# Performance work log

Hardware: AMD Instinct MI355X
Metric: run time of the kernel (lower is better)

Reference implementation:

```python
import jax, jax.numpy as jnp
import numpy as np

N = 4096
NFEAT = 1024
NHID = 512
NCLS = 32
NLAYERS = 3
SPARSITY = 0.002


def _l2norm(x, eps=1e-12):
    n = jnp.sqrt(jnp.sum(x * x, axis=1, keepdims=True))
    return x / jnp.maximum(n, eps)


def setup_inputs() -> dict:
    key = jax.random.key(0)
    ks = jax.random.split(key, 12)
    # sparse-valued dense adjacency (original stores torch.sparse but densifies every hop)
    vals = jax.random.uniform(ks[0], (N, N), dtype=jnp.float32)
    mask = jax.random.uniform(ks[1], (N, N)) < SPARSITY
    adj = jnp.where(mask, vals, 0.0)
    features = jax.random.normal(ks[2], (N, NFEAT), dtype=jnp.float32)
    # y is a one-hot label matrix [N, nclass]
    labels = jax.random.randint(ks[3], (N,), 0, NCLS)
    y = jax.nn.one_hot(labels, NCLS, dtype=jnp.float32)
    s = 0.02
    W0 = jax.random.normal(ks[4], (NFEAT + 3 * NCLS, NHID), dtype=jnp.float32) * s
    b0 = jnp.zeros((NHID,), jnp.float32)
    W1_0 = jax.random.normal(ks[5], (NHID + 3 * NCLS, NHID), dtype=jnp.float32) * s
    b1_0 = jnp.zeros((NHID,), jnp.float32)
    W1_1 = jax.random.normal(ks[6], (NHID + 3 * NCLS, NHID), dtype=jnp.float32) * s
    b1_1 = jnp.zeros((NHID,), jnp.float32)
    W2 = jax.random.normal(ks[7], (NFEAT + NHID, NCLS), dtype=jnp.float32) * s
    b2 = jnp.zeros((NCLS,), jnp.float32)
    alphas = jnp.ones((NLAYERS, 5), jnp.float32)
    return {
        "adj": adj, "features": features, "y": y,
        "W0": W0, "b0": b0, "W1_0": W1_0, "b1_0": b1_0,
        "W1_1": W1_1, "b1_1": b1_1, "W2": W2, "b2": b2,
        "alphas": alphas, "layer_norm": 1,
    }


def reference(adj, features, y, W0, b0, W1_0, b1_0, W1_1, b1_1, W2, b2, alphas, layer_norm):
    Ws = [(W0, b0), (W1_0, b1_0), (W1_1, b1_1)]
    initial_features = jax.lax.stop_gradient(features)  # .clone().detach()
    feats = features
    max_features = None
    pow_adj = adj  # persists across layers (faithful to original): hops adj, adj^2, adj^4
    for i in range(NLAYERS):
        mask_alpha = jax.nn.softmax(alphas[i], axis=0)
        for _ in range(i):
            pow_adj = adj @ pow_adj
        hop = pow_adj @ feats                                   # [N, d]
        dist = (pow_adj > 0).astype(adj.dtype)                  # binarized reachability
        y_out = dist @ y                                        # [N, c]
        y_in = dist.T @ y                                       # [N, c]
        y_all = y_in + y_out
        hop = mask_alpha[0] * hop
        y_out = mask_alpha[1] * y_out
        y_in = mask_alpha[2] * y_in
        y_all = mask_alpha[3] * y_all
        mat = jnp.concatenate([hop, y_out, y_in, y_all], axis=1)
        W, b = Ws[i]
        tmp = mat @ W + b
        if layer_norm:
            tmp = _l2norm(tmp)
        feats = tmp
        max_features = tmp if max_features is None else jnp.maximum(max_features, tmp)
    final_mat = jnp.concatenate([initial_features, max_features], axis=1)
    out = jax.nn.relu(final_mat)
    # dropout: eval mode (identity)
    out = out @ W2 + b2
    return jax.nn.log_softmax(out, axis=1)
```

## Files before the change

kernel.cpp:

```cpp
#include <hip/hip_runtime.h>
#include <hip/hip_bf16.h>
#include <math.h>

typedef unsigned long long u64;
typedef unsigned short ushort_t;
typedef float f32x4 __attribute__((ext_vector_type(4)));
typedef short s16x8 __attribute__((ext_vector_type(8)));

#define NN 4096
#define NF 1024
#define NH 512
#define NC 32
#define LDP 40

__device__ inline float bf2f(ushort_t u) {
    unsigned int v = ((unsigned int)u) << 16;
    return __uint_as_float(v);
}
__device__ inline ushort_t f2bf(float f) {
    __hip_bfloat16 h = __float2bfloat16(f);
    return *(ushort_t*)&h;
}

__device__ void role_build(int i, int l, const float* __restrict__ adj,
                           u64* __restrict__ B1, int* __restrict__ rowcnt,
                           int* __restrict__ colidx, float* __restrict__ vals) {
    const float* row = adj + (size_t)i * NN + l * 64;
    const float4* row4 = (const float4*)row;
    u64 w = 0;
    #pragma unroll
    for (int k = 0; k < 16; ++k) {
        float4 v = row4[k];
        if (v.x > 0.f) w |= 1ULL << (4*k + 0);
        if (v.y > 0.f) w |= 1ULL << (4*k + 1);
        if (v.z > 0.f) w |= 1ULL << (4*k + 2);
        if (v.w > 0.f) w |= 1ULL << (4*k + 3);
    }
    B1[(size_t)i*64 + l] = w;
    int cnt = __popcll(w);
    int pre = cnt;
    #pragma unroll
    for (int o = 1; o < 64; o <<= 1) {
        int u = __shfl_up(pre, o, 64);
        if (l >= o) pre += u;
    }
    int excl = pre - cnt;
    int total = __shfl(pre, 63, 64);
    u64 ww = w;
    int idx = excl;
    while (ww) {
        int b = __ffsll((unsigned long long)ww) - 1;
        ww &= ww - 1;
        if (idx < 64) {
            colidx[i*64 + idx] = l*64 + b;
            vals[i*64 + idx] = row[b];
        }
        ++idx;
    }
    int tot = total < 64 ? total : 64;
    for (int s = tot + l; s < 64; s += 64) {
        colidx[i*64 + s] = 0;
        vals[i*64 + s] = 0.f;
    }
    if (l == 0) {
        int r8 = (tot + 7) & ~7;
        rowcnt[i] = r8 < 64 ? r8 : 64;
    }
}

__device__ void role_wt(const float* __restrict__ W, ushort_t* __restrict__ Wt,
                        int ksrc0, int Kd, int idx, char* smem, int t) {
    float (*tile)[33] = (float(*)[33])smem;
    int ktiles = Kd >> 5;
    int kb = (idx % ktiles) * 32, nb = (idx / ktiles) * 32;
    int tc = t & 31, tr8 = t >> 5;
    for (int r = tr8; r < 32; r += 8)
        tile[r][tc] = W[(size_t)(ksrc0 + kb + r) * NH + nb + tc];
    __syncthreads();
    for (int r = tr8; r < 32; r += 8)
        Wt[(size_t)(nb + r) * Kd + kb + tc] = f2bf(tile[tc][r]);
}

__device__ void role_bsq(int i, int t, char* smem, const u64* __restrict__ Bidx,
                         const u64* __restrict__ Bdat, u64* __restrict__ Bout) {
    u64* ridx = (u64*)smem;
    u64* part = ridx + 64;
    int wid = t >> 6, lane = t & 63;
    if (t < 64) ridx[t] = Bidx[(size_t)i*64 + t];
    __syncthreads();
    u64 acc = 0;
    for (int u = wid*16; u < wid*16 + 16; ++u) {
        u64 w = ridx[u];
        while (w) {
            int k = u*64 + (__ffsll((unsigned long long)w) - 1);
            w &= (w - 1);
            acc |= Bdat[(size_t)k*64 + lane];
        }
    }
    part[wid*64 + lane] = acc;
    __syncthreads();
    if (t < 64) Bout[(size_t)i*64 + t] = part[t] | part[64+t] | part[128+t] | part[192+t];
}

__device__ void role_btrans(int tb, int wid, int l, char* smem,
                            const u64* __restrict__ B, u64* __restrict__ BT) {
    u64* ld = ((u64*)smem) + wid*64;
    int I = tb >> 6, J = tb & 63;
    ld[l] = B[(size_t)(I*64 + l)*64 + J];
    __syncthreads();
    u64 out = 0;
    #pragma unroll
    for (int r = 0; r < 64; ++r) out |= ((ld[r] >> l) & 1ULL) << r;
    BT[(size_t)(J*64 + l)*64 + I] = out;
}

__device__ void role_ymat(int rb, int t, char* smem, const u64* __restrict__ B,
                          const u64* __restrict__ BT, const u64* __restrict__ LC,
                          const float* __restrict__ asp, ushort_t* __restrict__ yc) {
    u64* LCt   = (u64*)smem;
    u64* rows  = LCt + 64*32;
    u64* rowsT = rows + 8*64;
    for (int k = t; k < 2048; k += 256) {
        int c = k >> 6, w = k & 63;
        LCt[w*32 + c] = LC[k];
    }
    for (int k = t; k < 512; k += 256) {
        int r = k >> 6, w = k & 63;
        rows[r*64 + w]  = B[(size_t)(rb + r)*64 + w];
        rowsT[r*64 + w] = BT[(size_t)(rb + r)*64 + w];
    }
    __syncthreads();
    int wid = t >> 6, lane = t & 63;
    int h = lane >> 5, c = lane & 31;
    int r = wid * 2 + h;
    int co = 0, ci = 0;
    #pragma unroll
    for (int w = 0; w < 64; ++w) {
        u64 lc = LCt[w*32 + c];
        co += __popcll(rows[r*64 + w]  & lc);
        ci += __popcll(rowsT[r*64 + w] & lc);
    }
    float a1 = asp[1], a2 = asp[2], a3 = asp[3];
    size_t i = rb + r;
    yc[i*96 + c]      = f2bf(a1 * (float)co);
    yc[i*96 + 32 + c] = f2bf(a2 * (float)ci);
    yc[i*96 + 64 + c] = f2bf(a3 * (float)(co + ci));
}

__device__ void role_gemm(int bx, int tid, char* smem, const ushort_t* __restrict__ Abf,
                          const float* __restrict__ Af, int Ka,
                          const ushort_t* __restrict__ Bt, int K,
                          ushort_t* __restrict__ Cb, float* __restrict__ Cf) {
    ushort_t* As = (ushort_t*)smem;
    ushort_t* Bs = As + 64*LDP;
    int xcd = bx & 7, rest = bx >> 3;
    int nt = rest & 7, mt = (rest >> 3) * 8 + xcd;
    int bm = mt * 64, bn = nt * 64;
    int srow = tid >> 2, scol = (tid & 3) * 8;
    int wid = tid >> 6, lane = tid & 63;
    int fr = lane & 15, hi2 = lane >> 4, fk = hi2 * 8;
    f32x4 acc[4] = {{0,0,0,0},{0,0,0,0},{0,0,0,0},{0,0,0,0}};
    for (int k0 = 0; k0 < K; k0 += 32) {
        if (Abf) {
            *(s16x8*)&As[srow * LDP + scol] =
                *(const s16x8*)&Abf[(size_t)(bm + srow) * Ka + k0 + scol];
        } else {
            const float* ap = &Af[(size_t)(bm + srow) * Ka + k0 + scol];
            float4 a0 = *(const float4*)ap;
            float4 a1 = *(const float4*)(ap + 4);
            s16x8 o;
            o[0] = (short)f2bf(a0.x); o[1] = (short)f2bf(a0.y);
            o[2] = (short)f2bf(a0.z); o[3] = (short)f2bf(a0.w);
            o[4] = (short)f2bf(a1.x); o[5] = (short)f2bf(a1.y);
            o[6] = (short)f2bf(a1.z); o[7] = (short)f2bf(a1.w);
            *(s16x8*)&As[srow * LDP + scol] = o;
        }
        *(s16x8*)&Bs[srow * LDP + scol] =
            *(const s16x8*)&Bt[(size_t)(bn + srow) * K + k0 + scol];
        __syncthreads();
        s16x8 af = *(const s16x8*)&As[(wid * 16 + fr) * LDP + fk];
        #pragma unroll
        for (int j = 0; j < 4; ++j) {
            s16x8 bfv = *(const s16x8*)&Bs[(j * 16 + fr) * LDP + fk];
            acc[j] = __builtin_amdgcn_mfma_f32_16x16x32_bf16(af, bfv, acc[j], 0, 0, 0);
        }
        __syncthreads();
    }
    int drow = bm + wid * 16 + hi2 * 4;
    #pragma unroll
    for (int j = 0; j < 4; ++j) {
        int col = bn + j * 16 + fr;
        #pragma unroll
        for (int r = 0; r < 4; ++r) {
            if (Cb) Cb[(size_t)(drow + r) * NH + col] = f2bf(acc[j][r]);
            else    Cf[(size_t)(drow + r) * NH + col] = acc[j][r];
        }
    }
}

__device__ void role_spmm(int i, int lane, const int* __restrict__ rc,
                          const int* __restrict__ ci, const float* __restrict__ vl,
                          const ushort_t* __restrict__ X, ushort_t* __restrict__ Y) {
    int cnt = rc[i];
    float acc[8] = {0,0,0,0,0,0,0,0};
    for (int p = 0; p < cnt; p += 8) {
        int4   c0 = *(const int4*)&ci[i*64 + p];
        int4   c1 = *(const int4*)&ci[i*64 + p + 4];
        float4 v0 = *(const float4*)&vl[i*64 + p];
        float4 v1 = *(const float4*)&vl[i*64 + p + 4];
        s16x8 x0 = *(const s16x8*)&X[(size_t)c0.x * NH + 8*lane];
        s16x8 x1 = *(const s16x8*)&X[(size_t)c0.y * NH + 8*lane];
        s16x8 x2 = *(const s16x8*)&X[(size_t)c0.z * NH + 8*lane];
        s16x8 x3 = *(const s16x8*)&X[(size_t)c0.w * NH + 8*lane];
        s16x8 x4 = *(const s16x8*)&X[(size_t)c1.x * NH + 8*lane];
        s16x8 x5 = *(const s16x8*)&X[(size_t)c1.y * NH + 8*lane];
        s16x8 x6 = *(const s16x8*)&X[(size_t)c1.z * NH + 8*lane];
        s16x8 x7 = *(const s16x8*)&X[(size_t)c1.w * NH + 8*lane];
        #pragma unroll
        for (int j = 0; j < 8; ++j) {
            acc[j] += v0.x * bf2f((ushort_t)x0[j]);
            acc[j] += v0.y * bf2f((ushort_t)x1[j]);
            acc[j] += v0.z * bf2f((ushort_t)x2[j]);
            acc[j] += v0.w * bf2f((ushort_t)x3[j]);
            acc[j] += v1.x * bf2f((ushort_t)x4[j]);
            acc[j] += v1.y * bf2f((ushort_t)x5[j]);
            acc[j] += v1.z * bf2f((ushort_t)x6[j]);
            acc[j] += v1.w * bf2f((ushort_t)x7[j]);
        }
    }
    s16x8 o;
    #pragma unroll
    for (int j = 0; j < 8; ++j) o[j] = (short)f2bf(acc[j]);
    *(s16x8*)&Y[(size_t)i*NH + 8*lane] = o;
}

__device__ void role_spmmF(int i, int lane, const int* __restrict__ rc,
                           const int* __restrict__ ci, const float* __restrict__ vl,
                           const ushort_t* __restrict__ X, const float* __restrict__ yv,
                           const float* __restrict__ bias, int ln, float alpha,
                           ushort_t* __restrict__ F) {
    int cnt = rc[i];
    float acc[8] = {0,0,0,0,0,0,0,0};
    for (int p = 0; p < cnt; p += 8) {
        int4   c0 = *(const int4*)&ci[i*64 + p];
        int4   c1 = *(const int4*)&ci[i*64 + p + 4];
        float4 v0 = *(const float4*)&vl[i*64 + p];
        float4 v1 = *(const float4*)&vl[i*64 + p + 4];
        s16x8 x0 = *(const s16x8*)&X[(size_t)c0.x * NH + 8*lane];
        s16x8 x1 = *(const s16x8*)&X[(size_t)c0.y * NH + 8*lane];
        s16x8 x2 = *(const s16x8*)&X[(size_t)c0.z * NH + 8*lane];
        s16x8 x3 = *(const s16x8*)&X[(size_t)c0.w * NH + 8*lane];
        s16x8 x4 = *(const s16x8*)&X[(size_t)c1.x * NH + 8*lane];
        s16x8 x5 = *(const s16x8*)&X[(size_t)c1.y * NH + 8*lane];
        s16x8 x6 = *(const s16x8*)&X[(size_t)c1.z * NH + 8*lane];
        s16x8 x7 = *(const s16x8*)&X[(size_t)c1.w * NH + 8*lane];
        #pragma unroll
        for (int j = 0; j < 8; ++j) {
            acc[j] += v0.x * bf2f((ushort_t)x0[j]);
            acc[j] += v0.y * bf2f((ushort_t)x1[j]);
            acc[j] += v0.z * bf2f((ushort_t)x2[j]);
            acc[j] += v0.w * bf2f((ushort_t)x3[j]);
            acc[j] += v1.x * bf2f((ushort_t)x4[j]);
            acc[j] += v1.y * bf2f((ushort_t)x5[j]);
            acc[j] += v1.z * bf2f((ushort_t)x6[j]);
            acc[j] += v1.w * bf2f((ushort_t)x7[j]);
        }
    }
    const float* yr = yv + (size_t)i * NH + 8*lane;
    float4 ya = *(const float4*)yr;
    float4 yb = *(const float4*)(yr + 4);
    float4 ba = *(const float4*)&bias[8*lane];
    float4 bb = *(const float4*)&bias[8*lane + 4];
    float v[8];
    v[0] = alpha*acc[0] + ya.x + ba.x; v[1] = alpha*acc[1] + ya.y + ba.y;
    v[2] = alpha*acc[2] + ya.z + ba.z; v[3] = alpha*acc[3] + ya.w + ba.w;
    v[4] = alpha*acc[4] + yb.x + bb.x; v[5] = alpha*acc[5] + yb.y + bb.y;
    v[6] = alpha*acc[6] + yb.z + bb.z; v[7] = alpha*acc[7] + yb.w + bb.w;
    float ss = 0.f;
    #pragma unroll
    for (int j = 0; j < 8; ++j) ss += v[j]*v[j];
    #pragma unroll
    for (int o = 1; o < 64; o <<= 1) ss += __shfl_xor(ss, o, 64);
    float sc = ln ? 1.0f / fmaxf(sqrtf(ss), 1e-12f) : 1.0f;
    s16x8 o;
    #pragma unroll
    for (int j = 0; j < 8; ++j) o[j] = (short)f2bf(v[j] * sc);
    *(s16x8*)&F[(size_t)i*NH + 8*lane] = o;
}

__global__ __launch_bounds__(256) void k_setup(const float* __restrict__ adj,
        const float* __restrict__ y, u64* __restrict__ LC,
        const float* __restrict__ W0, const float* __restrict__ W1_0,
        const float* __restrict__ W1_1,
        ushort_t* __restrict__ Wh0t, ushort_t* __restrict__ Wy0t,
        ushort_t* __restrict__ Wh1t, ushort_t* __restrict__ Wy1t,
        ushort_t* __restrict__ Wh2t, ushort_t* __restrict__ Wy2t,
        const float* __restrict__ alphas, float* __restrict__ a_sm,
        u64* __restrict__ B1, int* __restrict__ rowcnt,
        int* __restrict__ colidx, float* __restrict__ vals) {
    __shared__ __align__(16) char smem[4352];
    int b = blockIdx.x, t = threadIdx.x;
    int wid = t >> 6, l = t & 63;
    if (b < 1024) {
        role_build(b*4 + wid, l, adj, B1, rowcnt, colidx, vals);
    } else if (b < 1040) {
        int w = (b - 1024) * 4 + wid;
        const float* yr = y + (size_t)(w*64 + l) * NC;
        for (int c = 0; c < NC; ++c) {
            u64 m = __ballot(yr[c] > 0.5f);
            if (l == c) LC[c*64 + w] = m;
        }
    } else if (b < 1552) { role_wt(W0,   Wh0t, 0,    NF, b - 1040, smem, t); }
    else if (b < 1600)   { role_wt(W0,   Wy0t, NF,   96, b - 1552, smem, t); }
    else if (b < 1856)   { role_wt(W1_0, Wh1t, 0,    NH, b - 1600, smem, t); }
    else if (b < 1904)   { role_wt(W1_0, Wy1t, NH,   96, b - 1856, smem, t); }
    else if (b < 2160)   { role_wt(W1_1, Wh2t, 0,    NH, b - 1904, smem, t); }
    else if (b < 2208)   { role_wt(W1_1, Wy2t, NH,   96, b - 2160, smem, t); }
    else {
        if (t == 0) {
            for (int i = 0; i < 3; ++i) {
                float m = -1e30f;
                for (int j = 0; j < 5; ++j) m = fmaxf(m, alphas[i*5+j]);
                float e[5]; float s = 0.f;
                for (int j = 0; j < 5; ++j) { e[j] = expf(alphas[i*5+j] - m); s += e[j]; }
                for (int j = 0; j < 5; ++j) a_sm[i*5+j] = e[j] / s;
            }
        }
    }
}

__global__ __launch_bounds__(256) void k_p2(const float* __restrict__ features,
        const ushort_t* __restrict__ Wh0t, ushort_t* __restrict__ zb,
        const u64* __restrict__ B1, u64* __restrict__ B2, u64* __restrict__ B1T) {
    __shared__ __align__(16) char smem[10240];
    int b = blockIdx.x, t = threadIdx.x;
    int wid = t >> 6, l = t & 63;
    if (b < 512)       role_gemm(b, t, smem, nullptr, features, NF, Wh0t, NF, zb, nullptr);
    else if (b < 4608) role_bsq(b - 512, t, smem, B1, B1, B2);
    else               role_btrans((b - 4608)*4 + wid, wid, l, smem, B1, B1T);
}

__global__ __launch_bounds__(256) void k_p3(const u64* __restrict__ B1,
        const u64* __restrict__ B2, u64* __restrict__ B3, u64* __restrict__ B2T,
        const u64* __restrict__ B1T, const u64* __restrict__ LC,
        const float* __restrict__ a_sm, ushort_t* __restrict__ y0c) {
    __shared__ __align__(16) char smem[24576];
    int b = blockIdx.x, t = threadIdx.x;
    int wid = t >> 6, l = t & 63;
    if (b < 4096)      role_bsq(b, t, smem, B1, B2, B3);
    else if (b < 5120) role_btrans((b - 4096)*4 + wid, wid, l, smem, B2, B2T);
    else               role_ymat((b - 5120)*8, t, smem, B1, B1T, LC, a_sm, y0c);
}

__global__ __launch_bounds__(256) void k_p4(const ushort_t* __restrict__ y0c,
        const ushort_t* __restrict__ Wy0t, float* __restrict__ yv0,
        const u64* __restrict__ B2, const u64* __restrict__ B2T,
        const u64* __restrict__ LC, const float* __restrict__ a_sm,
        ushort_t* __restrict__ y1c,
        const u64* __restrict__ B1, const u64* __restrict__ B3, u64* __restrict__ B4) {
    __shared__ __align__(16) char smem[24576];
    int b = blockIdx.x, t = threadIdx.x;
    if (b < 512)       role_gemm(b, t, smem, y0c, nullptr, 96, Wy0t, 96, nullptr, yv0);
    else if (b < 1024) role_ymat((b - 512)*8, t, smem, B2, B2T, LC, a_sm + 5, y1c);
    else               role_bsq(b - 1024, t, smem, B1, B3, B4);
}

__global__ __launch_bounds__(256) void k_p5(const int* __restrict__ rc,
        const int* __restrict__ ci, const float* __restrict__ vl,
        const ushort_t* __restrict__ zb, const float* __restrict__ yv0,
        const float* __restrict__ b0, const int* __restrict__ lnflag,
        const float* __restrict__ a_sm, ushort_t* __restrict__ f1,
        const u64* __restrict__ B4, u64* __restrict__ B4T,
        const ushort_t* __restrict__ y1c, const ushort_t* __restrict__ Wy1t,
        float* __restrict__ yv1) {
    __shared__ __align__(16) char smem[10240];
    int b = blockIdx.x, t = threadIdx.x;
    int wid = t >> 6, l = t & 63;
    if (b < 1024)
        role_spmmF(b*4 + wid, l, rc, ci, vl, zb, yv0, b0, *lnflag, a_sm[0], f1);
    else if (b < 2048)
        role_btrans((b - 1024)*4 + wid, wid, l, smem, B4, B4T);
    else
        role_gemm(b - 2048, t, smem, y1c, nullptr, 96, Wy1t, 96, nullptr, yv1);
}

__global__ __launch_bounds__(256) void k_p6(const ushort_t* __restrict__ f1,
        const ushort_t* __restrict__ Wh1t, ushort_t* __restrict__ zb,
        const u64* __restrict__ B4, const u64* __restrict__ B4T,
        const u64* __restrict__ LC, const float* __restrict__ a_sm,
        ushort_t* __restrict__ y2c) {
    __shared__ __align__(16) char smem[24576];
    int b = blockIdx.x, t = threadIdx.x;
    if (b < 512) role_gemm(b, t, smem, f1, nullptr, NH, Wh1t, NH, zb, nullptr);
    else         role_ymat((b - 512)*8, t, smem, B4, B4T, LC, a_sm + 10, y2c);
}

__global__ __launch_bounds__(256) void k_p7(const int* __restrict__ rc,
        const int* __restrict__ ci, const float* __restrict__ vl,
        const ushort_t* __restrict__ zb, ushort_t* __restrict__ ub,
        const ushort_t* __restrict__ y2c, const ushort_t* __restrict__ Wy2t,
        float* __restrict__ yv2) {
    __shared__ __align__(16) char smem[10240];
    int b = blockIdx.x, t = threadIdx.x;
    int wid = t >> 6, l = t & 63;
    if (b < 1024) role_spmm(b*4 + wid, l, rc, ci, vl, zb, ub);
    else          role_gemm(b - 1024, t, smem, y2c, nullptr, 96, Wy2t, 96, nullptr, yv2);
}

__global__ __launch_bounds__(256) void k_spmm(const int* __restrict__ rc,
        const int* __restrict__ ci, const float* __restrict__ vl,
        const ushort_t* __restrict__ X, ushort_t* __restrict__ Y) {
    role_spmm(blockIdx.x*4 + (threadIdx.x >> 6), threadIdx.x & 63, rc, ci, vl, X, Y);
}

__global__ __launch_bounds__(256) void k_spmmF(const int* __restrict__ rc,
        const int* __restrict__ ci, const float* __restrict__ vl,
        const ushort_t* __restrict__ X, const float* __restrict__ yv,
        const float* __restrict__ bias, const int* __restrict__ lnflag,
        const float* __restrict__ a_sm, int ai, ushort_t* __restrict__ F) {
    role_spmmF(blockIdx.x*4 + (threadIdx.x >> 6), threadIdx.x & 63, rc, ci, vl,
               X, yv, bias, *lnflag, a_sm[ai], F);
}

__global__ __launch_bounds__(256) void k_gemmz(const ushort_t* __restrict__ A,
        const ushort_t* __restrict__ Bt, ushort_t* __restrict__ C, int K) {
    __shared__ __align__(16) char smem[10240];
    role_gemm(blockIdx.x, threadIdx.x, smem, A, nullptr, K, Bt, K, C, nullptr);
}

__global__ __launch_bounds__(256) void k_final(const float* __restrict__ feat0,
        const ushort_t* __restrict__ f1, const ushort_t* __restrict__ f2,
        const ushort_t* __restrict__ f3, const float* __restrict__ W2,
        const float* __restrict__ b2, float* __restrict__ out) {
    int rb = blockIdx.x * 8;
    int t = threadIdx.x;
    __shared__ float rows[8][NF + NH];
    __shared__ float part[8][8][32];
    #pragma unroll
    for (int r = 0; r < 8; ++r) {
        const float* f0 = feat0 + (size_t)(rb + r) * NF;
        float4 v = *(const float4*)&f0[t * 4];
        rows[r][t*4+0] = fmaxf(v.x, 0.f);
        rows[r][t*4+1] = fmaxf(v.y, 0.f);
        rows[r][t*4+2] = fmaxf(v.z, 0.f);
        rows[r][t*4+3] = fmaxf(v.w, 0.f);
    }
    #pragma unroll
    for (int q = 0; q < 2; ++q) {
        int ch = t*2 + q;
        int rr = ch >> 6, k8 = (ch & 63) * 8;
        s16x8 a = *(const s16x8*)&f1[(size_t)(rb + rr)*NH + k8];
        s16x8 bq = *(const s16x8*)&f2[(size_t)(rb + rr)*NH + k8];
        s16x8 cq = *(const s16x8*)&f3[(size_t)(rb + rr)*NH + k8];
        #pragma unroll
        for (int j = 0; j < 8; ++j) {
            float m = fmaxf(fmaxf(bf2f((ushort_t)a[j]), bf2f((ushort_t)bq[j])),
                            bf2f((ushort_t)cq[j]));
            rows[rr][NF + k8 + j] = fmaxf(m, 0.f);
        }
    }
    __syncthreads();
    int c = t & 31, g = t >> 5;
    float acc[8] = {0,0,0,0,0,0,0,0};
    for (int k = g * 192; k < (g + 1) * 192; ++k) {
        float w = W2[(size_t)k * NC + c];
        #pragma unroll
        for (int r = 0; r < 8; ++r) acc[r] += rows[r][k] * w;
    }
    #pragma unroll
    for (int r = 0; r < 8; ++r) part[g][r][c] = acc[r];
    __syncthreads();
    int r = g;
    float lg = b2[c];
    #pragma unroll
    for (int gg = 0; gg < 8; ++gg) lg += part[gg][r][c];
    float m = lg;
    #pragma unroll
    for (int o = 16; o > 0; o >>= 1) m = fmaxf(m, __shfl_xor(m, o, 32));
    float e = expf(lg - m), s = e;
    #pragma unroll
    for (int o = 16; o > 0; o >>= 1) s += __shfl_xor(s, o, 32);
    out[(size_t)(rb + r) * NC + c] = lg - m - logf(s);
}

extern "C" void kernel_launch(void* const* d_in, const int* in_sizes, int n_in,
                              void* d_out, int out_size, void* d_ws, size_t ws_size,
                              hipStream_t stream) {
    const float* adj      = (const float*)d_in[0];
    const float* features = (const float*)d_in[1];
    const float* y        = (const float*)d_in[2];
    const float* W0       = (const float*)d_in[3];
    const float* b0       = (const float*)d_in[4];
    const float* W1_0     = (const float*)d_in[5];
    const float* b1_0     = (const float*)d_in[6];
    const float* W1_1     = (const float*)d_in[7];
    const float* b1_1     = (const float*)d_in[8];
    const float* W2       = (const float*)d_in[9];
    const float* b2       = (const float*)d_in[10];
    const float* alphas   = (const float*)d_in[11];
    const int*   lnflag   = (const int*)d_in[12];
    float* out = (float*)d_out;

    char* ws = (char*)d_ws;
    size_t off = 0;
    auto alloc = [&](size_t bytes) -> char* {
        char* p = ws + off;
        off = (off + bytes + 255) & ~(size_t)255;
        return p;
    };
    float* a_sm   = (float*)alloc(16 * 4);
    int*   rowcnt = (int*)alloc((size_t)NN * 4);
    int*   colidx = (int*)alloc((size_t)NN * 64 * 4);
    float* vals   = (float*)alloc((size_t)NN * 64 * 4);
    u64* B1  = (u64*)alloc((size_t)NN * 64 * 8);
    u64* B2  = (u64*)alloc((size_t)NN * 64 * 8);
    u64* B3  = (u64*)alloc((size_t)NN * 64 * 8);
    u64* B4  = (u64*)alloc((size_t)NN * 64 * 8);
    u64* B1T = (u64*)alloc((size_t)NN * 64 * 8);
    u64* B2T = (u64*)alloc((size_t)NN * 64 * 8);
    u64* B4T = (u64*)alloc((size_t)NN * 64 * 8);
    u64* LC  = (u64*)alloc((size_t)NC * 64 * 8);
    ushort_t* Wh0t = (ushort_t*)alloc((size_t)NH * NF * 2);
    ushort_t* Wh1t = (ushort_t*)alloc((size_t)NH * NH * 2);
    ushort_t* Wh2t = (ushort_t*)alloc((size_t)NH * NH * 2);
    ushort_t* Wy0t = (ushort_t*)alloc((size_t)NH * 96 * 2);
    ushort_t* Wy1t = (ushort_t*)alloc((size_t)NH * 96 * 2);
    ushort_t* Wy2t = (ushort_t*)alloc((size_t)NH * 96 * 2);
    ushort_t* y0c  = (ushort_t*)alloc((size_t)NN * 96 * 2);
    ushort_t* y1c  = (ushort_t*)alloc((size_t)NN * 96 * 2);
    ushort_t* y2c  = (ushort_t*)alloc((size_t)NN * 96 * 2);
    float* yv0 = (float*)alloc((size_t)NN * NH * 4);
    float* yv1 = (float*)alloc((size_t)NN * NH * 4);
    float* yv2 = (float*)alloc((size_t)NN * NH * 4);
    ushort_t* zb = (ushort_t*)alloc((size_t)NN * NH * 2);
    ushort_t* ub = (ushort_t*)alloc((size_t)NN * NH * 2);
    ushort_t* vb = (ushort_t*)alloc((size_t)NN * NH * 2);
    ushort_t* f1 = (ushort_t*)alloc((size_t)NN * NH * 2);
    ushort_t* f2 = (ushort_t*)alloc((size_t)NN * NH * 2);
    ushort_t* f3 = (ushort_t*)alloc((size_t)NN * NH * 2);

    k_setup<<<2209, 256, 0, stream>>>(adj, y, LC, W0, W1_0, W1_1,
                                      Wh0t, Wy0t, Wh1t, Wy1t, Wh2t, Wy2t,
                                      alphas, a_sm, B1, rowcnt, colidx, vals);
    k_p2<<<5632, 256, 0, stream>>>(features, Wh0t, zb, B1, B2, B1T);
    k_p3<<<5632, 256, 0, stream>>>(B1, B2, B3, B2T, B1T, LC, a_sm, y0c);
    k_p4<<<5120, 256, 0, stream>>>(y0c, Wy0t, yv0, B2, B2T, LC, a_sm, y1c, B1, B3, B4);
    k_p5<<<2560, 256, 0, stream>>>(rowcnt, colidx, vals, zb, yv0, b0, lnflag, a_sm,
                                   f1, B4, B4T, y1c, Wy1t, yv1);
    k_p6<<<1024, 256, 0, stream>>>(f1, Wh1t, zb, B4, B4T, LC, a_sm, y2c);
    k_p7<<<1536, 256, 0, stream>>>(rowcnt, colidx, vals, zb, ub, y2c, Wy2t, yv2);
    k_spmmF<<<1024, 256, 0, stream>>>(rowcnt, colidx, vals, ub, yv1, b1_0, lnflag,
                                      a_sm, 5, f2);
    k_gemmz<<<512, 256, 0, stream>>>(f2, Wh2t, zb, NH);
    k_spmm<<<1024, 256, 0, stream>>>(rowcnt, colidx, vals, zb, ub);
    k_spmm<<<1024, 256, 0, stream>>>(rowcnt, colidx, vals, ub, vb);
    k_spmm<<<1024, 256, 0, stream>>>(rowcnt, colidx, vals, vb, ub);
    k_spmmF<<<1024, 256, 0, stream>>>(rowcnt, colidx, vals, ub, yv2, b1_1, lnflag,
                                      a_sm, 10, f3);
    k_final<<<512, 256, 0, stream>>>(features, f1, f2, f3, W2, b2, out);
}
```

Before: 195.3 us.

## Precompute sparse A^2 and reuse it to halve sparse hop passes

Builds an explicit sparse A^2 in ELL form (up to 128 entries per row) inside k_p2, then computes the layer-1 hop as A^2·Z and the layer-2 hop as A^2·(A^2·Z), replacing four A-SpMM passes with three A^2 passes. The binary reachability chain is shortened by squaring B2 directly to get B4 instead of going through B3, and the phase kernels are reshuffled so the k_p7 launch disappears. The cost is extra build work and denser rows per SpMM. Rows of A^2 with more than 128 nonzeros are silently truncated, and the row count is rounded up to 8 using zero padding.

```diff
diff --git a/kernel.cpp b/kernel.cpp
--- a/kernel.cpp
+++ b/kernel.cpp
@@ -112,6 +112,61 @@
     #pragma unroll
     for (int r = 0; r < 64; ++r) out |= ((ld[r] >> l) & 1ULL) << r;
     BT[(size_t)(J*64 + l)*64 + I] = out;
+}
+
+__device__ void role_a2build(int i, int t, char* smem, const int* __restrict__ rowcnt,
+                             const int* __restrict__ colidx, const float* __restrict__ vals,
+                             int* __restrict__ colidx2, float* __restrict__ vals2,
+                             int* __restrict__ rowcnt2) {
+    float* colacc = (float*)smem;
+    int* wcnt = (int*)(smem + 16384);
+    for (int k = t; k < 4096; k += 256) colacc[k] = 0.f;
+    __syncthreads();
+    int wid = t >> 6, l = t & 63;
+    int cti = rowcnt[i];
+    for (int p = 0; p < cti; ++p) {
+        int j = colidx[i*64 + p];
+        float vij = vals[i*64 + p];
+        int ctj = rowcnt[j];
+        if (l < ctj) {
+            int k = colidx[j*64 + l];
+            float vjk = vals[j*64 + l];
+            if ((k >> 10) == wid) colacc[k] += vij * vjk;
+        }
+    }
+    __syncthreads();
+    int cnt_w = 0;
+    for (int c = 0; c < 16; ++c) {
+        float v = colacc[wid*1024 + c*64 + l];
+        u64 mm = __ballot(v != 0.f);
+        cnt_w += __popcll(mm);
+    }
+    if (l == 0) wcnt[wid] = cnt_w;
+    __syncthreads();
+    int prefix = 0;
+    for (int wq = 0; wq < wid; ++wq) prefix += wcnt[wq];
+    int total = wcnt[0] + wcnt[1] + wcnt[2] + wcnt[3];
+    int pos = prefix;
+    for (int c = 0; c < 16; ++c) {
+        int col = wid*1024 + c*64 + l;
+        float v = colacc[col];
+        u64 mm = __ballot(v != 0.f);
+        if (v != 0.f) {
+            int off2 = __popcll(mm & ((1ULL << l) - 1ULL));
+            int s = pos + off2;
+            if (s < 128) { colidx2[(size_t)i*128 + s] = col; vals2[(size_t)i*128 + s] = v; }
+        }
+        pos += __popcll(mm);
+    }
+    int tot2 = total < 128 ? total : 128;
+    for (int s = tot2 + t; s < 128; s += 256) {
+        colidx2[(size_t)i*128 + s] = 0;
+        vals2[(size_t)i*128 + s] = 0.f;
+    }
+    if (t == 0) {
+        int r8 = (tot2 + 7) & ~7;
+        rowcnt2[i] = r8 < 128 ? r8 : 128;
+    }
 }
 
 __device__ void role_ymat(int rb, int t, char* smem, const u64* __restrict__ B,
@@ -200,14 +255,14 @@
 
 __device__ void role_spmm(int i, int lane, const int* __restrict__ rc,
                           const int* __restrict__ ci, const float* __restrict__ vl,
-                          const ushort_t* __restrict__ X, ushort_t* __restrict__ Y) {
+                          int cap, const ushort_t* __restrict__ X, ushort_t* __restrict__ Y) {
     int cnt = rc[i];
     float acc[8] = {0,0,0,0,0,0,0,0};
     for (int p = 0; p < cnt; p += 8) {
-        int4   c0 = *(const int4*)&ci[i*64 + p];
-        int4   c1 = *(const int4*)&ci[i*64 + p + 4];
-        float4 v0 = *(const float4*)&vl[i*64 + p];
-        float4 v1 = *(const float4*)&vl[i*64 + p + 4];
+        int4   c0 = *(const int4*)&ci[(size_t)i*cap + p];
+        int4   c1 = *(const int4*)&ci[(size_t)i*cap + p + 4];
+        float4 v0 = *(const float4*)&vl[(size_t)i*cap + p];
+        float4 v1 = *(const float4*)&vl[(size_t)i*cap + p + 4];
         s16x8 x0 = *(const s16x8*)&X[(size_t)c0.x * NH + 8*lane];
         s16x8 x1 = *(const s16x8*)&X[(size_t)c0.y * NH + 8*lane];
         s16x8 x2 = *(const s16x8*)&X[(size_t)c0.z * NH + 8*lane];
@@ -236,16 +291,17 @@
 
 __device__ void role_spmmF(int i, int lane, const int* __restrict__ rc,
                            const int* __restrict__ ci, const float* __restrict__ vl,
-                           const ushort_t* __restrict__ X, const float* __restrict__ yv,
+                           int cap, const ushort_t* __restrict__ X,
+                           const float* __restrict__ yv,
                            const float* __restrict__ bias, int ln, float alpha,
                            ushort_t* __restrict__ F) {
     int cnt = rc[i];
     float acc[8] = {0,0,0,0,0,0,0,0};
     for (int p = 0; p < cnt; p += 8) {
-        int4   c0 = *(const int4*)&ci[i*64 + p];
-        int4   c1 = *(const int4*)&ci[i*64 + p + 4];
-        float4 v0 = *(const float4*)&vl[i*64 + p];
-        float4 v1 = *(const float4*)&vl[i*64 + p + 4];
+        int4   c0 = *(const int4*)&ci[(size_t)i*cap + p];
+        int4   c1 = *(const int4*)&ci[(size_t)i*cap + p + 4];
+        float4 v0 = *(const float4*)&vl[(size_t)i*cap + p];
+        float4 v1 = *(const float4*)&vl[(size_t)i*cap + p + 4];
         s16x8 x0 = *(const s16x8*)&X[(size_t)c0.x * NH + 8*lane];
         s16x8 x1 = *(const s16x8*)&X[(size_t)c0.y * NH + 8*lane];
         s16x8 x2 = *(const s16x8*)&X[(size_t)c0.z * NH + 8*lane];
@@ -331,23 +387,28 @@
 
 __global__ __launch_bounds__(256) void k_p2(const float* __restrict__ features,
         const ushort_t* __restrict__ Wh0t, ushort_t* __restrict__ zb,
-        const u64* __restrict__ B1, u64* __restrict__ B2, u64* __restrict__ B1T) {
-    __shared__ __align__(16) char smem[10240];
+        const u64* __restrict__ B1, u64* __restrict__ B2, u64* __restrict__ B1T,
+        const int* __restrict__ rowcnt, const int* __restrict__ colidx,
+        const float* __restrict__ vals,
+        int* __restrict__ colidx2, float* __restrict__ vals2, int* __restrict__ rowcnt2) {
+    __shared__ __align__(16) char smem[16512];
     int b = blockIdx.x, t = threadIdx.x;
     int wid = t >> 6, l = t & 63;
     if (b < 512)       role_gemm(b, t, smem, nullptr, features, NF, Wh0t, NF, zb, nullptr);
     else if (b < 4608) role_bsq(b - 512, t, smem, B1, B1, B2);
-    else               role_btrans((b - 4608)*4 + wid, wid, l, smem, B1, B1T);
+    else if (b < 5632) role_btrans((b - 4608)*4 + wid, wid, l, smem, B1, B1T);
+    else               role_a2build(b - 5632, t, smem, rowcnt, colidx, vals,
+                                    colidx2, vals2, rowcnt2);
 }
 
 __global__ __launch_bounds__(256) void k_p3(const u64* __restrict__ B1,
-        const u64* __restrict__ B2, u64* __restrict__ B3, u64* __restrict__ B2T,
+        const u64* __restrict__ B2, u64* __restrict__ B4, u64* __restrict__ B2T,
         const u64* __restrict__ B1T, const u64* __restrict__ LC,
         const float* __restrict__ a_sm, ushort_t* __restrict__ y0c) {
     __shared__ __align__(16) char smem[24576];
     int b = blockIdx.x, t = threadIdx.x;
     int wid = t >> 6, l = t & 63;
-    if (b < 4096)      role_bsq(b, t, smem, B1, B2, B3);
+    if (b < 4096)      role_bsq(b, t, smem, B2, B2, B4);
     else if (b < 5120) role_btrans((b - 4096)*4 + wid, wid, l, smem, B2, B2T);
     else               role_ymat((b - 5120)*8, t, smem, B1, B1T, LC, a_sm, y0c);
 }
@@ -357,12 +418,13 @@
         const u64* __restrict__ B2, const u64* __restrict__ B2T,
         const u64* __restrict__ LC, const float* __restrict__ a_sm,
         ushort_t* __restrict__ y1c,
-        const u64* __restrict__ B1, const u64* __restrict__ B3, u64* __restrict__ B4) {
+        const u64* __restrict__ B4, u64* __restrict__ B4T) {
     __shared__ __align__(16) char smem[24576];
     int b = blockIdx.x, t = threadIdx.x;
+    int wid = t >> 6, l = t & 63;
     if (b < 512)       role_gemm(b, t, smem, y0c, nullptr, 96, Wy0t, 96, nullptr, yv0);
     else if (b < 1024) role_ymat((b - 512)*8, t, smem, B2, B2T, LC, a_sm + 5, y1c);
-    else               role_bsq(b - 1024, t, smem, B1, B3, B4);
+    else               role_btrans((b - 1024)*4 + wid, wid, l, smem, B4, B4T);
 }
 
 __global__ __launch_bounds__(256) void k_p5(const int* __restrict__ rc,
@@ -370,55 +432,43 @@
         const ushort_t* __restrict__ zb, const float* __restrict__ yv0,
         const float* __restrict__ b0, const int* __restrict__ lnflag,
         const float* __restrict__ a_sm, ushort_t* __restrict__ f1,
-        const u64* __restrict__ B4, u64* __restrict__ B4T,
         const ushort_t* __restrict__ y1c, const ushort_t* __restrict__ Wy1t,
-        float* __restrict__ yv1) {
-    __shared__ __align__(16) char smem[10240];
+        float* __restrict__ yv1,
+        const u64* __restrict__ B4, const u64* __restrict__ B4T,
+        const u64* __restrict__ LC, ushort_t* __restrict__ y2c) {
+    __shared__ __align__(16) char smem[24576];
     int b = blockIdx.x, t = threadIdx.x;
     int wid = t >> 6, l = t & 63;
     if (b < 1024)
-        role_spmmF(b*4 + wid, l, rc, ci, vl, zb, yv0, b0, *lnflag, a_sm[0], f1);
-    else if (b < 2048)
-        role_btrans((b - 1024)*4 + wid, wid, l, smem, B4, B4T);
+        role_spmmF(b*4 + wid, l, rc, ci, vl, 64, zb, yv0, b0, *lnflag, a_sm[0], f1);
+    else if (b < 1536)
+        role_gemm(b - 1024, t, smem, y1c, nullptr, 96, Wy1t, 96, nullptr, yv1);
     else
-        role_gemm(b - 2048, t, smem, y1c, nullptr, 96, Wy1t, 96, nullptr, yv1);
+        role_ymat((b - 1536)*8, t, smem, B4, B4T, LC, a_sm + 10, y2c);
 }
 
 __global__ __launch_bounds__(256) void k_p6(const ushort_t* __restrict__ f1,
         const ushort_t* __restrict__ Wh1t, ushort_t* __restrict__ zb,
-        const u64* __restrict__ B4, const u64* __restrict__ B4T,
-        const u64* __restrict__ LC, const float* __restrict__ a_sm,
-        ushort_t* __restrict__ y2c) {
-    __shared__ __align__(16) char smem[24576];
-    int b = blockIdx.x, t = threadIdx.x;
-    if (b < 512) role_gemm(b, t, smem, f1, nullptr, NH, Wh1t, NH, zb, nullptr);
-    else         role_ymat((b - 512)*8, t, smem, B4, B4T, LC, a_sm + 10, y2c);
-}
-
-__global__ __launch_bounds__(256) void k_p7(const int* __restrict__ rc,
-        const int* __restrict__ ci, const float* __restrict__ vl,
-        const ushort_t* __restrict__ zb, ushort_t* __restrict__ ub,
         const ushort_t* __restrict__ y2c, const ushort_t* __restrict__ Wy2t,
         float* __restrict__ yv2) {
     __shared__ __align__(16) char smem[10240];
     int b = blockIdx.x, t = threadIdx.x;
-    int wid = t >> 6, l = t & 63;
-    if (b < 1024) role_spmm(b*4 + wid, l, rc, ci, vl, zb, ub);
-    else          role_gemm(b - 1024, t, smem, y2c, nullptr, 96, Wy2t, 96, nullptr, yv2);
-}
-
-__global__ __launch_bounds__(256) void k_spmm(const int* __restrict__ rc,
+    if (b < 512) role_gemm(b, t, smem, f1, nullptr, NH, Wh1t, NH, zb, nullptr);
+    else         role_gemm(b - 512, t, smem, y2c, nullptr, 96, Wy2t, 96, nullptr, yv2);
+}
+
+__global__ __launch_bounds__(256) void k_spmm2(const int* __restrict__ rc,
         const int* __restrict__ ci, const float* __restrict__ vl,
         const ushort_t* __restrict__ X, ushort_t* __restrict__ Y) {
-    role_spmm(blockIdx.x*4 + (threadIdx.x >> 6), threadIdx.x & 63, rc, ci, vl, X, Y);
-}
-
-__global__ __launch_bounds__(256) void k_spmmF(const int* __restrict__ rc,
+    role_spmm(blockIdx.x*4 + (threadIdx.x >> 6), threadIdx.x & 63, rc, ci, vl, 128, X, Y);
+}
+
+__global__ __launch_bounds__(256) void k_spmmF2(const int* __restrict__ rc,
         const int* __restrict__ ci, const float* __restrict__ vl,
         const ushort_t* __restrict__ X, const float* __restrict__ yv,
         const float* __restrict__ bias, const int* __restrict__ lnflag,
         const float* __restrict__ a_sm, int ai, ushort_t* __restrict__ F) {
-    role_spmmF(blockIdx.x*4 + (threadIdx.x >> 6), threadIdx.x & 63, rc, ci, vl,
+    role_spmmF(blockIdx.x*4 + (threadIdx.x >> 6), threadIdx.x & 63, rc, ci, vl, 128,
                X, yv, bias, *lnflag, a_sm[ai], F);
 }
 
@@ -508,13 +558,15 @@
         off = (off + bytes + 255) & ~(size_t)255;
         return p;
     };
-    float* a_sm   = (float*)alloc(16 * 4);
-    int*   rowcnt = (int*)alloc((size_t)NN * 4);
-    int*   colidx = (int*)alloc((size_t)NN * 64 * 4);
-    float* vals   = (float*)alloc((size_t)NN * 64 * 4);
+    float* a_sm    = (float*)alloc(16 * 4);
+    int*   rowcnt  = (int*)alloc((size_t)NN * 4);
+    int*   colidx  = (int*)alloc((size_t)NN * 64 * 4);
+    float* vals    = (float*)alloc((size_t)NN * 64 * 4);
+    int*   rowcnt2 = (int*)alloc((size_t)NN * 4);
+    int*   colidx2 = (int*)alloc((size_t)NN * 128 * 4);
+    float* vals2   = (float*)alloc((size_t)NN * 128 * 4);
     u64* B1  = (u64*)alloc((size_t)NN * 64 * 8);
     u64* B2  = (u64*)alloc((size_t)NN * 64 * 8);
-    u64* B3  = (u64*)alloc((size_t)NN * 64 * 8);
     u64* B4  = (u64*)alloc((size_t)NN * 64 * 8);
     u64* B1T = (u64*)alloc((size_t)NN * 64 * 8);
     u64* B2T = (u64*)alloc((size_t)NN * 64 * 8);
@@ -534,7 +586,6 @@
     float* yv2 = (float*)alloc((size_t)NN * NH * 4);
     ushort_t* zb = (ushort_t*)alloc((size_t)NN * NH * 2);
     ushort_t* ub = (ushort_t*)alloc((size_t)NN * NH * 2);
-    ushort_t* vb = (ushort_t*)alloc((size_t)NN * NH * 2);
     ushort_t* f1 = (ushort_t*)alloc((size_t)NN * NH * 2);
     ushort_t* f2 = (ushort_t*)alloc((size_t)NN * NH * 2);
     ushort_t* f3 = (ushort_t*)alloc((size_t)NN * NH * 2);
@@ -542,20 +593,18 @@
     k_setup<<<2209, 256, 0, stream>>>(adj, y, LC, W0, W1_0, W1_1,
                                       Wh0t, Wy0t, Wh1t, Wy1t, Wh2t, Wy2t,
                                       alphas, a_sm, B1, rowcnt, colidx, vals);
-    k_p2<<<5632, 256, 0, stream>>>(features, Wh0t, zb, B1, B2, B1T);
-    k_p3<<<5632, 256, 0, stream>>>(B1, B2, B3, B2T, B1T, LC, a_sm, y0c);
-    k_p4<<<5120, 256, 0, stream>>>(y0c, Wy0t, yv0, B2, B2T, LC, a_sm, y1c, B1, B3, B4);
-    k_p5<<<2560, 256, 0, stream>>>(rowcnt, colidx, vals, zb, yv0, b0, lnflag, a_sm,
-                                   f1, B4, B4T, y1c, Wy1t, yv1);
-    k_p6<<<1024, 256, 0, stream>>>(f1, Wh1t, zb, B4, B4T, LC, a_sm, y2c);
-    k_p7<<<1536, 256, 0, stream>>>(rowcnt, colidx, vals, zb, ub, y2c, Wy2t, yv2);
-    k_spmmF<<<1024, 256, 0, stream>>>(rowcnt, colidx, vals, ub, yv1, b1_0, lnflag,
-                                      a_sm, 5, f2);
+    k_p2<<<9728, 256, 0, stream>>>(features, Wh0t, zb, B1, B2, B1T,
+                                   rowcnt, colidx, vals, colidx2, vals2, rowcnt2);
+    k_p3<<<5632, 256, 0, stream>>>(B1, B2, B4, B2T, B1T, LC, a_sm, y0c);
+    k_p4<<<2048, 256, 0, stream>>>(y0c, Wy0t, yv0, B2, B2T, LC, a_sm, y1c, B4, B4T);
+    k_p5<<<2048, 256, 0, stream>>>(rowcnt, colidx, vals, zb, yv0, b0, lnflag, a_sm,
+                                   f1, y1c, Wy1t, yv1, B4, B4T, LC, y2c);
+    k_p6<<<1024, 256, 0, stream>>>(f1, Wh1t, zb, y2c, Wy2t, yv2);
+    k_spmmF2<<<1024, 256, 0, stream>>>(rowcnt2, colidx2, vals2, zb, yv1, b1_0, lnflag,
+                                       a_sm, 5, f2);
     k_gemmz<<<512, 256, 0, stream>>>(f2, Wh2t, zb, NH);
-    k_spmm<<<1024, 256, 0, stream>>>(rowcnt, colidx, vals, zb, ub);
-    k_spmm<<<1024, 256, 0, stream>>>(rowcnt, colidx, vals, ub, vb);
-    k_spmm<<<1024, 256, 0, stream>>>(rowcnt, colidx, vals, vb, ub);
-    k_spmmF<<<1024, 256, 0, stream>>>(rowcnt, colidx, vals, ub, yv2, b1_1, lnflag,
-                                      a_sm, 10, f3);
+    k_spmm2<<<1024, 256, 0, stream>>>(rowcnt2, colidx2, vals2, zb, ub);
+    k_spmmF2<<<1024, 256, 0, stream>>>(rowcnt2, colidx2, vals2, ub, yv2, b1_1, lnflag,
+                                       a_sm, 10, f3);
     k_final<<<512, 256, 0, stream>>>(features, f1, f2, f3, W2, b2, out);
 }
```

Measured after the change: 242.3 us. 24.1% more time.
